# Optimization experiments

Measured on AMD Instinct MI355X. Metric: run time of the kernel, lower is better.

## Reference

```python
import jax, jax.numpy as jnp
import numpy as np

B, N, P, K, C = 8, 4096, 4096, 32, 128  # batch, points, npoint, neighbors, channels (=mlp[-1])
W_OUT = 16  # weightnet output channels (from Linear(16*mlp[-1], mlp[-1]))
EPS = 1e-5


def setup_inputs() -> dict:
    key = jax.random.key(0)
    ks = jax.random.split(key, 9)
    xyz = jax.random.normal(ks[0], (B, P, 3), jnp.float32)
    points = jax.random.normal(ks[1], (B, N, C), jnp.float32)
    local_coordinates = jax.random.normal(ks[2], (B, P, K, 3), jnp.float32)
    neighbor_lists = jax.random.randint(ks[3], (B, P, K), 0, N)
    data_idx = jax.random.randint(ks[4], (B,), 0, B)
    Ww = jax.random.normal(ks[5], (3, W_OUT), jnp.float32) * 0.1   # weightnet (pointwise linear 3->16)
    bw = jnp.zeros((W_OUT,), jnp.float32)
    Wl = jax.random.normal(ks[6], (W_OUT * C, C), jnp.float32) * 0.02  # nn.Linear(16*mlp[-1], mlp[-1])
    bl = jnp.zeros((C,), jnp.float32)
    gamma = jnp.ones((C,), jnp.float32)   # BatchNorm1d weight
    beta = jnp.zeros((C,), jnp.float32)   # BatchNorm1d bias
    return {"xyz": xyz, "points": points, "local_coordinates": local_coordinates,
            "neighbor_lists": neighbor_lists, "data_idx": data_idx,
            "Ww": Ww, "bw": bw, "Wl": Wl, "bl": bl, "gamma": gamma, "beta": beta}


def reference(xyz, points, local_coordinates, neighbor_lists, data_idx, Ww, bw, Wl, bl, gamma, beta):
    b, p, k, _ = local_coordinates.shape
    c = points.shape[-1]
    # weightnet: pointwise map of 3-D local coordinates to 16 weight channels -> [B,P,K,16]
    weights = local_coordinates @ Ww + bw
    # irregular neighbor gather: data[b,p,k,:] = points[b, neighbor_lists[b,p,k], :] -> [B,P,K,C]
    data = points[jnp.arange(b)[:, None, None], neighbor_lists]
    # per-point weighted aggregation over K neighbors: [B,P,C,16] -> flatten to [B,P,C*16]
    new_points = jnp.einsum('bpkc,bpkw->bpcw', data, weights).reshape(b, p, c * weights.shape[-1])
    # batch reindex via data_idx
    new_points = new_points[data_idx]
    # linear tail: [B,P,C]
    new_points = new_points @ Wl + bl
    # BatchNorm1d over channel dim (training-mode batch stats), then ReLU: [B,C,P]
    x = new_points.transpose(0, 2, 1)
    mean = x.mean(axis=(0, 2), keepdims=True)
    var = x.var(axis=(0, 2), keepdims=True)
    x = (x - mean) * jax.lax.rsqrt(var + EPS) * gamma[None, :, None] + beta[None, :, None]
    return xyz, jax.nn.relu(x)
```

## Files before the change

### kernel.cpp

```cpp
#include <hip/hip_runtime.h>

#define Bn 8
#define Nn 4096
#define Pn 4096
#define Kn 32
#define Cn 128

using float4v = __attribute__((ext_vector_type(4))) float;
using short8  = __attribute__((ext_vector_type(8))) short;

__device__ __forceinline__ unsigned short bf16b(float f) {
  union { float f; unsigned u; } v; v.f = f;
  unsigned r = v.u + 0x7FFFu + ((v.u >> 16) & 1u);
  return (unsigned short)(r >> 16);
}

__device__ __forceinline__ unsigned pkhi(float x, float y) {
  return __builtin_amdgcn_perm(__float_as_uint(y), __float_as_uint(x), 0x07060302u);
}

__device__ __forceinline__ void gld_lds16(const void* g, void* l) {
  __builtin_amdgcn_global_load_lds(
      (const __attribute__((address_space(1))) unsigned int*)g,
      (__attribute__((address_space(3))) unsigned int*)l, 16, 0, 0);
}

__global__ __launch_bounds__(256) void prep(const float* __restrict__ Wl,
                                            unsigned short* __restrict__ WlT,
                                            const float* __restrict__ xyz,
                                            float* __restrict__ out,
                                            float* __restrict__ gacc) {
  __shared__ unsigned short tile[128 * 130];
  const int t = threadIdx.x, blk = blockIdx.x;
  if (blk < 16) {
#pragma unroll
    for (int i = 0; i < 64; ++i) {
      int idx = i * 256 + t;
      int kl = idx >> 7, n = idx & 127;
      tile[n * 130 + kl] = bf16b(Wl[(size_t)(blk * 128 + kl) * 128 + n]);
    }
    __syncthreads();
#pragma unroll
    for (int i = 0; i < 64; ++i) {
      int idx = i * 256 + t;
      int n = idx >> 7, kl = idx & 127;
      WlT[(size_t)n * 2048 + blk * 128 + kl] = tile[n * 130 + kl];
    }
  } else {
    if (blk == 16) gacc[t] = 0.f;
    const int i0 = (blk - 16) * 3072 + t * 12;
#pragma unroll
    for (int i = 0; i < 3; ++i)
      *(float4v*)(out + i0 + i * 4) = *(const float4v*)(xyz + i0 + i * 4);
  }
}

__global__ __launch_bounds__(64) void stage1(
    const float* __restrict__ points, const float* __restrict__ lc,
    const int* __restrict__ nl, const int* __restrict__ didx,
    const float* __restrict__ Ww, const float* __restrict__ bwv,
    unsigned short* __restrict__ Mglob) {
  __shared__ unsigned short slab[32 * 128];

  const int lane = threadIdx.x;
  const int l15 = lane & 15, q = lane >> 4;
  const int b = blockIdx.x & 7;
  const int pg = blockIdx.x >> 3;
  const int db = didx[b];
  const float2* __restrict__ pbat2 =
      (const float2*)(points + (size_t)db * Nn * Cn);
  const float Ww0 = Ww[l15], Ww1 = Ww[16 + l15], Ww2 = Ww[32 + l15];
  const float bw0 = bwv[l15];

  for (int pi = 0; pi < 4; ++pi) {
    const int p = pg * 4 + pi;
    const unsigned pk = (unsigned)((db * Pn + p) * Kn);
    int nk[32];
    const int4* __restrict__ nl4 = (const int4*)(nl + pk);
#pragma unroll
    for (int i = 0; i < 8; ++i) *(int4*)&nk[i * 4] = nl4[i];
    const float* __restrict__ lcp = lc + (size_t)(pk + q * 8) * 3;
    float la[24];
#pragma unroll
    for (int v = 0; v < 6; ++v) *(float4v*)&la[v * 4] = *(const float4v*)(lcp + v * 4);
    short8 af;
#pragma unroll
    for (int j = 0; j < 8; ++j) {
      float w = bw0 + la[3 * j] * Ww0 + la[3 * j + 1] * Ww1 + la[3 * j + 2] * Ww2;
      af[j] = (short)bf16b(w);
    }
    __builtin_amdgcn_wave_barrier();
#pragma unroll
    for (int r = 0; r < 32; ++r) {
      const float2 v = pbat2[((unsigned)nk[r] << 6) + lane];
      const unsigned idx = r * 128 + ((lane * 2 + (r >> 3) * 16) & 127);
      *(unsigned*)&slab[idx] = pkhi(v.x, v.y);
    }
    __builtin_amdgcn_wave_barrier();
    const unsigned moff = ((unsigned)(b * Pn + p)) << 11;
#pragma unroll
    for (int ct = 0; ct < 8; ++ct) {
      const int coff = (ct * 16 + l15 + q * 16) & 127;
      short8 bfv;
#pragma unroll
      for (int j = 0; j < 8; ++j)
        bfv[j] = (short)slab[(q * 8 + j) * 128 + coff];
      float4v d = {0.f, 0.f, 0.f, 0.f};
      d = __builtin_amdgcn_mfma_f32_16x16x32_bf16(af, bfv, d, 0, 0, 0);
      uint2 u;
      u.x = pkhi(d[0], d[1]);
      u.y = pkhi(d[2], d[3]);
      *(uint2*)&Mglob[moff + (ct * 16 + l15) * 16 + q * 4] = u;
    }
    __builtin_amdgcn_wave_barrier();
  }
}

__global__ __launch_bounds__(256) void stage2(
    const unsigned short* __restrict__ Mglob,
    const unsigned short* __restrict__ WlT, const float* __restrict__ blv,
    float* __restrict__ xout, float* __restrict__ gacc) {
  __shared__ unsigned short As[32 * 64];
  __shared__ unsigned short Bs[128 * 64];
  __shared__ float red[256];

  const int t = threadIdx.x, lane = t & 63, wave = t >> 6;
  const int l15 = lane & 15, q = lane >> 4;
  const int lr = lane >> 3, lchk = lane & 7;
  const int bidx = blockIdx.x & 7;
  const int pt0 = (blockIdx.x >> 3) * 32;
  const size_t row0 = (size_t)bidx * Pn + pt0;

  float4v acc[2][2];
#pragma unroll
  for (int rt = 0; rt < 2; ++rt)
#pragma unroll
    for (int nt = 0; nt < 2; ++nt) acc[rt][nt] = (float4v){0.f, 0.f, 0.f, 0.f};

  for (int kk = 0; kk < 32; ++kk) {
    const int k0 = kk * 64;
    gld_lds16(Mglob + (row0 + wave * 8 + lr) * 2048 + k0 + (lchk ^ lr) * 8,
              &As[wave * 8 * 64]);
#pragma unroll
    for (int it = 0; it < 4; ++it) {
      const int n = wave * 32 + it * 8 + lr;
      gld_lds16(WlT + (size_t)n * 2048 + k0 + (lchk ^ lr) * 8,
                &Bs[(wave * 32 + it * 8) * 64]);
    }
    __syncthreads();
#pragma unroll
    for (int ks = 0; ks < 2; ++ks) {
      short8 a[2], bq[2];
#pragma unroll
      for (int rt = 0; rt < 2; ++rt) {
        const int row = rt * 16 + l15;
        a[rt] = *(const short8*)&As[row * 64 + (((ks * 4 + q) ^ (row & 7)) << 3)];
      }
#pragma unroll
      for (int nt = 0; nt < 2; ++nt) {
        const int n = wave * 32 + nt * 16 + l15;
        bq[nt] = *(const short8*)&Bs[n * 64 + (((ks * 4 + q) ^ (n & 7)) << 3)];
      }
#pragma unroll
      for (int rt = 0; rt < 2; ++rt)
#pragma unroll
        for (int nt = 0; nt < 2; ++nt)
          acc[rt][nt] = __builtin_amdgcn_mfma_f32_16x16x32_bf16(a[rt], bq[nt],
                                                                acc[rt][nt], 0, 0, 0);
    }
    __syncthreads();
  }

#pragma unroll
  for (int nt = 0; nt < 2; ++nt) {
    const int ch = wave * 32 + nt * 16 + l15;
    const float bb = blv[ch];
    float s = 0.f, sq = 0.f;
#pragma unroll
    for (int rt = 0; rt < 2; ++rt) {
      float4v o;
#pragma unroll
      for (int r = 0; r < 4; ++r) {
        float v = acc[rt][nt][r] + bb; o[r] = v; s += v; sq += v * v;
      }
      *(float4v*)(xout + ((size_t)bidx * Cn + ch) * Pn + pt0 + rt * 16 + q * 4) = o;
    }
    s += __shfl_xor(s, 16); s += __shfl_xor(s, 32);
    sq += __shfl_xor(sq, 16); sq += __shfl_xor(sq, 32);
    if (lane < 16) { red[ch] = s; red[128 + ch] = sq; }
  }
  __syncthreads();
  atomicAdd(&gacc[t], red[t]);
}

__global__ __launch_bounds__(256) void finalize_ln(float* __restrict__ x,
                                                   const float* __restrict__ gacc,
                                                   const float* __restrict__ gamma,
                                                   const float* __restrict__ beta) {
  const int idx = blockIdx.x * 256 + threadIdx.x;
  const int fi = idx * 4;
  const int c = (fi >> 12) & 127;
  const float inv = 1.f / 32768.f;
  const float mean = gacc[c] * inv;
  const float var = gacc[128 + c] * inv - mean * mean;
  const float scale = rsqrtf(var + 1e-5f) * gamma[c];
  const float shift = beta[c] - mean * scale;
  float4v v = *(float4v*)(x + fi);
#pragma unroll
  for (int r = 0; r < 4; ++r) v[r] = fmaxf(v[r] * scale + shift, 0.f);
  *(float4v*)(x + fi) = v;
}

extern "C" void kernel_launch(void* const* d_in, const int* in_sizes, int n_in,
                              void* d_out, int out_size, void* d_ws, size_t ws_size,
                              hipStream_t stream) {
  const float* xyz    = (const float*)d_in[0];
  const float* points = (const float*)d_in[1];
  const float* lc     = (const float*)d_in[2];
  const int*   nl     = (const int*)d_in[3];
  const int*   didx   = (const int*)d_in[4];
  const float* Ww     = (const float*)d_in[5];
  const float* bw     = (const float*)d_in[6];
  const float* Wl     = (const float*)d_in[7];
  const float* bl     = (const float*)d_in[8];
  const float* gamma  = (const float*)d_in[9];
  const float* beta   = (const float*)d_in[10];

  float* out  = (float*)d_out;
  float* xout = out + (size_t)Bn * Pn * 3;
  unsigned short* WlT = (unsigned short*)d_ws;
  float* gacc = (float*)((char*)d_ws + (size_t)512 * 1024);
  unsigned short* Mglob =
      (unsigned short*)((char*)d_ws + (size_t)1024 * 1024);

  prep<<<48, 256, 0, stream>>>(Wl, WlT, xyz, out, gacc);
  stage1<<<8192, 64, 0, stream>>>(points, lc, nl, didx, Ww, bw, Mglob);
  stage2<<<1024, 256, 0, stream>>>(Mglob, WlT, bl, xout, gacc);
  finalize_ln<<<4096, 256, 0, stream>>>(xout, gacc, gamma, beta);
}
```

Before: 212.4 us.

## Fuse gather-aggregation stage into linear GEMM kernel per 32-point tile

Measured after the change: 214.1 us. Within noise of the previous version (+0.8%).

```diff
diff --git a/kernel.cpp b/kernel.cpp
--- a/kernel.cpp
+++ b/kernel.cpp
@@ -55,80 +55,80 @@
   }
 }
 
-__global__ __launch_bounds__(64) void stage1(
+__global__ __launch_bounds__(256) void unified(
     const float* __restrict__ points, const float* __restrict__ lc,
     const int* __restrict__ nl, const int* __restrict__ didx,
     const float* __restrict__ Ww, const float* __restrict__ bwv,
-    unsigned short* __restrict__ Mglob) {
-  __shared__ unsigned short slab[32 * 128];
-
-  const int lane = threadIdx.x;
-  const int l15 = lane & 15, q = lane >> 4;
-  const int b = blockIdx.x & 7;
-  const int pg = blockIdx.x >> 3;
-  const int db = didx[b];
-  const float2* __restrict__ pbat2 =
-      (const float2*)(points + (size_t)db * Nn * Cn);
-  const float Ww0 = Ww[l15], Ww1 = Ww[16 + l15], Ww2 = Ww[32 + l15];
-  const float bw0 = bwv[l15];
-
-  for (int pi = 0; pi < 4; ++pi) {
-    const int p = pg * 4 + pi;
-    const unsigned pk = (unsigned)((db * Pn + p) * Kn);
-    int nk[32];
-    const int4* __restrict__ nl4 = (const int4*)(nl + pk);
-#pragma unroll
-    for (int i = 0; i < 8; ++i) *(int4*)&nk[i * 4] = nl4[i];
-    const float* __restrict__ lcp = lc + (size_t)(pk + q * 8) * 3;
-    float la[24];
-#pragma unroll
-    for (int v = 0; v < 6; ++v) *(float4v*)&la[v * 4] = *(const float4v*)(lcp + v * 4);
-    short8 af;
-#pragma unroll
-    for (int j = 0; j < 8; ++j) {
-      float w = bw0 + la[3 * j] * Ww0 + la[3 * j + 1] * Ww1 + la[3 * j + 2] * Ww2;
-      af[j] = (short)bf16b(w);
-    }
-    __builtin_amdgcn_wave_barrier();
-#pragma unroll
-    for (int r = 0; r < 32; ++r) {
-      const float2 v = pbat2[((unsigned)nk[r] << 6) + lane];
-      const unsigned idx = r * 128 + ((lane * 2 + (r >> 3) * 16) & 127);
-      *(unsigned*)&slab[idx] = pkhi(v.x, v.y);
-    }
-    __builtin_amdgcn_wave_barrier();
-    const unsigned moff = ((unsigned)(b * Pn + p)) << 11;
-#pragma unroll
-    for (int ct = 0; ct < 8; ++ct) {
-      const int coff = (ct * 16 + l15 + q * 16) & 127;
-      short8 bfv;
-#pragma unroll
-      for (int j = 0; j < 8; ++j)
-        bfv[j] = (short)slab[(q * 8 + j) * 128 + coff];
-      float4v d = {0.f, 0.f, 0.f, 0.f};
-      d = __builtin_amdgcn_mfma_f32_16x16x32_bf16(af, bfv, d, 0, 0, 0);
-      uint2 u;
-      u.x = pkhi(d[0], d[1]);
-      u.y = pkhi(d[2], d[3]);
-      *(uint2*)&Mglob[moff + (ct * 16 + l15) * 16 + q * 4] = u;
-    }
-    __builtin_amdgcn_wave_barrier();
-  }
-}
-
-__global__ __launch_bounds__(256) void stage2(
-    const unsigned short* __restrict__ Mglob,
+    unsigned short* __restrict__ Mglob,
     const unsigned short* __restrict__ WlT, const float* __restrict__ blv,
     float* __restrict__ xout, float* __restrict__ gacc) {
-  __shared__ unsigned short As[32 * 64];
-  __shared__ unsigned short Bs[128 * 64];
-  __shared__ float red[256];
+  __shared__ __align__(16) unsigned char smem[32768];
 
   const int t = threadIdx.x, lane = t & 63, wave = t >> 6;
   const int l15 = lane & 15, q = lane >> 4;
-  const int lr = lane >> 3, lchk = lane & 7;
   const int bidx = blockIdx.x & 7;
   const int pt0 = (blockIdx.x >> 3) * 32;
+  const int db = didx[bidx];
+
+  {
+    unsigned short* __restrict__ slab =
+        (unsigned short*)smem + wave * 4096;
+    const float2* __restrict__ pbat2 =
+        (const float2*)(points + (size_t)db * Nn * Cn);
+    const float Ww0 = Ww[l15], Ww1 = Ww[16 + l15], Ww2 = Ww[32 + l15];
+    const float bw0 = bwv[l15];
+
+    for (int pi = 0; pi < 8; ++pi) {
+      const int p = pt0 + wave * 8 + pi;
+      const unsigned pk = (unsigned)((db * Pn + p) * Kn);
+      int nk[32];
+      const int4* __restrict__ nl4 = (const int4*)(nl + pk);
+#pragma unroll
+      for (int i = 0; i < 8; ++i) *(int4*)&nk[i * 4] = nl4[i];
+      const float* __restrict__ lcp = lc + (size_t)(pk + q * 8) * 3;
+      float la[24];
+#pragma unroll
+      for (int v = 0; v < 6; ++v)
+        *(float4v*)&la[v * 4] = *(const float4v*)(lcp + v * 4);
+      short8 af;
+#pragma unroll
+      for (int j = 0; j < 8; ++j) {
+        float w = bw0 + la[3 * j] * Ww0 + la[3 * j + 1] * Ww1 + la[3 * j + 2] * Ww2;
+        af[j] = (short)bf16b(w);
+      }
+      __builtin_amdgcn_wave_barrier();
+#pragma unroll
+      for (int r = 0; r < 32; ++r) {
+        const float2 v = pbat2[((unsigned)nk[r] << 6) + lane];
+        const unsigned idx = r * 128 + ((lane * 2 + (r >> 3) * 16) & 127);
+        *(unsigned*)&slab[idx] = pkhi(v.x, v.y);
+      }
+      __builtin_amdgcn_wave_barrier();
+      const unsigned moff = ((unsigned)(bidx * Pn + p)) << 11;
+#pragma unroll
+      for (int ct = 0; ct < 8; ++ct) {
+        const int coff = (ct * 16 + l15 + q * 16) & 127;
+        short8 bfv;
+#pragma unroll
+        for (int j = 0; j < 8; ++j)
+          bfv[j] = (short)slab[(q * 8 + j) * 128 + coff];
+        float4v d = {0.f, 0.f, 0.f, 0.f};
+        d = __builtin_amdgcn_mfma_f32_16x16x32_bf16(af, bfv, d, 0, 0, 0);
+        uint2 u;
+        u.x = pkhi(d[0], d[1]);
+        u.y = pkhi(d[2], d[3]);
+        *(uint2*)&Mglob[moff + (ct * 16 + l15) * 16 + q * 4] = u;
+      }
+      __builtin_amdgcn_wave_barrier();
+    }
+  }
+  __syncthreads();
+
+  unsigned short* __restrict__ As = (unsigned short*)smem;
+  unsigned short* __restrict__ Bs = (unsigned short*)smem + 2048;
+  float* __restrict__ red = (float*)((unsigned short*)smem + 10240);
+
+  const int lr = lane >> 3, lchk = lane & 7;
   const size_t row0 = (size_t)bidx * Pn + pt0;
 
   float4v acc[2][2];
@@ -234,7 +234,7 @@
       (unsigned short*)((char*)d_ws + (size_t)1024 * 1024);
 
   prep<<<48, 256, 0, stream>>>(Wl, WlT, xyz, out, gacc);
-  stage1<<<8192, 64, 0, stream>>>(points, lc, nl, didx, Ww, bw, Mglob);
-  stage2<<<1024, 256, 0, stream>>>(Mglob, WlT, bl, xout, gacc);
+  unified<<<1024, 256, 0, stream>>>(points, lc, nl, didx, Ww, bw, Mglob,
+                                    WlT, bl, xout, gacc);
   finalize_ln<<<4096, 256, 0, stream>>>(xout, gacc, gamma, beta);
 }
```
